# Optimization experiments

Hardware: AMD Instinct MI355X
Metric: run time of the kernel (lower is better)

## Reference

```python
import jax, jax.numpy as jnp
import numpy as np

IN_CH = 512
HID = 512
SCALE = 1.0 / np.sqrt(16.0)  # hard-coded 16**0.5 in source, not sqrt(hidden)


def setup_inputs() -> dict:
    key = jax.random.key(0)
    ks = jax.random.split(key, 9)
    B, T = 8, 2048
    lim = 1.0 / np.sqrt(IN_CH)
    return {
        "q": jax.random.normal(ks[0], (B, T, IN_CH), dtype=jnp.float32),
        "k": jax.random.normal(ks[1], (B, T, IN_CH), dtype=jnp.float32),
        "v": jax.random.normal(ks[2], (B, T, IN_CH), dtype=jnp.float32),
        "Wq": jax.random.uniform(ks[3], (IN_CH, HID), jnp.float32, -lim, lim),
        "bq": jax.random.uniform(ks[4], (HID,), jnp.float32, -lim, lim),
        "Wk": jax.random.uniform(ks[5], (IN_CH, HID), jnp.float32, -lim, lim),
        "bk": jax.random.uniform(ks[6], (HID,), jnp.float32, -lim, lim),
        "Wv": jax.random.uniform(ks[7], (IN_CH, HID), jnp.float32, -lim, lim),
        "bv": jax.random.uniform(ks[8], (HID,), jnp.float32, -lim, lim),
    }


def reference(q, k, v, Wq, bq, Wk, bk, Wv, bv):
    # Linear projections: [B,T,F] @ [F,H] + [H]
    query = jnp.einsum("btf,fh->bth", q, Wq) + bq
    key_p = jnp.einsum("btf,fh->bth", k, Wk) + bk
    value = jnp.einsum("btf,fh->bth", v, Wv) + bv
    # energy: [B,T,T], scaled by fixed 1/sqrt(16)
    energy = jnp.einsum("bth,bsh->bts", query, key_p) * SCALE
    attn = jax.nn.softmax(energy, axis=-1)
    # weighted sum: [B,T,H]
    return jnp.einsum("bts,bsh->bth", attn, value)
```

## Files before the change

### kernel.cpp

```cpp
#include <hip/hip_runtime.h>
#include <stdint.h>

typedef __bf16 bf16;
typedef bf16 bf16x8 __attribute__((ext_vector_type(8)));
typedef float f32x4 __attribute__((ext_vector_type(4)));

#define MFMA(a, b, c) __builtin_amdgcn_mfma_f32_16x16x32_bf16(a, b, c, 0, 0, 0)

#define SCALE_L2E 0.3606737602222409f
#define M0 16.0f

__device__ __forceinline__ void gload_lds16(const void* g, void* l) {
  __builtin_amdgcn_global_load_lds(
      (const __attribute__((address_space(1))) uint32_t*)g,
      (__attribute__((address_space(3))) uint32_t*)l, 16, 0, 0);
}

__global__ void k_wtrans(const float* __restrict__ Wq, const float* __restrict__ Wk,
                         const float* __restrict__ Wv, bf16* __restrict__ Wt) {
  __shared__ float tile[32][33];
  int x = threadIdx.x, y = threadIdx.y;
  int k0 = blockIdx.x * 32, n0 = blockIdx.y * 32, z = blockIdx.z;
  const float* W = (z == 0) ? Wq : (z == 1) ? Wk : Wv;
  for (int j = 0; j < 4; j++)
    tile[y + 8 * j][x] = W[(size_t)(k0 + y + 8 * j) * 512 + n0 + x];
  __syncthreads();
  bf16* o = Wt + (size_t)z * 262144;
  for (int j = 0; j < 4; j++)
    o[(size_t)(n0 + y + 8 * j) * 512 + k0 + x] = (bf16)tile[x][y + 8 * j];
}

__global__ __launch_bounds__(256, 3) void k_proj(
    const float* __restrict__ q, const float* __restrict__ k, const float* __restrict__ v,
    const bf16* __restrict__ Wt, const float* __restrict__ bq, const float* __restrict__ bk,
    const float* __restrict__ bv, bf16* __restrict__ Qp, bf16* __restrict__ Kp,
    bf16* __restrict__ Vtp) {
  int z = blockIdx.z;
  const float* A = (z == 0) ? q : (z == 1) ? k : v;
  const float* bias = (z == 0) ? bq : (z == 1) ? bk : bv;
  const bf16* Bw = Wt + (size_t)z * 262144;

  int m0 = blockIdx.x * 128, n0 = blockIdx.y * 128;
  __shared__ __align__(16) char smem[34816];
  bf16* As = (bf16*)smem;
  bf16* Bs = (bf16*)(smem + 18432);
  bf16* Ts = (bf16*)smem;

  int tid = threadIdx.x;
  int wave = tid >> 6, lane = tid & 63, qr = lane & 15, quad = lane >> 4;
  int wm = (wave >> 1) * 64, wn = (wave & 1) * 64;

  f32x4 acc[4][4];
  for (int mi = 0; mi < 4; mi++)
    for (int ni = 0; ni < 4; ni++) acc[mi][ni] = (f32x4){0.f, 0.f, 0.f, 0.f};

  for (int k0 = 0; k0 < 512; k0 += 64) {
    __syncthreads();
    for (int i = 0; i < 4; i++) {
      int ch = i * 256 + tid;
      int row = ch >> 3, c = ch & 7;
      int cs = c ^ (row & 7);
      gload_lds16(Bw + (size_t)(n0 + row) * 512 + k0 + cs * 8, &Bs[ch * 8]);
      const float4* src = (const float4*)(A + (size_t)(m0 + row) * 512 + k0 + c * 8);
      float4 x = src[0], y = src[1];
      bf16x8 t;
      t[0] = (bf16)x.x; t[1] = (bf16)x.y; t[2] = (bf16)x.z; t[3] = (bf16)x.w;
      t[4] = (bf16)y.x; t[5] = (bf16)y.y; t[6] = (bf16)y.z; t[7] = (bf16)y.w;
      *(bf16x8*)&As[row * 72 + c * 8] = t;
    }
    __syncthreads();
    for (int h = 0; h < 2; h++) {
      bf16x8 af[4], bfv[4];
      for (int mi = 0; mi < 4; mi++)
        af[mi] = *(bf16x8*)&As[(wm + mi * 16 + qr) * 72 + h * 32 + quad * 8];
      for (int ni = 0; ni < 4; ni++) {
        int rr = wn + ni * 16 + qr;
        int cc = (h * 4 + quad) ^ (rr & 7);
        bfv[ni] = *(bf16x8*)&Bs[rr * 64 + cc * 8];
      }
      for (int mi = 0; mi < 4; mi++)
        for (int ni = 0; ni < 4; ni++) acc[mi][ni] = MFMA(af[mi], bfv[ni], acc[mi][ni]);
    }
  }

  if (z == 2) {
    __syncthreads();
    for (int ni = 0; ni < 4; ni++) {
      int hcol = wn + ni * 16 + qr;
      float bz = bias[n0 + hcol];
      for (int mi = 0; mi < 4; mi++) {
        int tl = wm + mi * 16 + quad * 4;
        bf16 tmp[4];
        for (int r = 0; r < 4; r++) tmp[r] = (bf16)(acc[mi][ni][r] + bz);
        *(uint64_t*)&Ts[hcol * 136 + tl] = *(uint64_t*)tmp;
      }
    }
    __syncthreads();
    int bb = m0 >> 11, t0l = m0 & 2047;
    for (int i = 0; i < 8; i++) {
      int ch = i * 256 + tid;
      int row = ch >> 4, c = ch & 15;
      *(bf16x8*)(Vtp + (size_t)(bb * 512 + n0 + row) * 2048 + t0l + c * 8) =
          *(bf16x8*)&Ts[row * 136 + c * 8];
    }
  } else {
    bf16* C = (z == 0) ? Qp : Kp;
    float sc = (z == 0) ? SCALE_L2E : 1.0f;
    for (int ni = 0; ni < 4; ni++) {
      int col = n0 + wn + ni * 16 + qr;
      float bz = bias[col];
      for (int mi = 0; mi < 4; mi++) {
        int rbase = m0 + wm + mi * 16 + quad * 4;
        for (int r = 0; r < 4; r++)
          C[(size_t)(rbase + r) * 512 + col] = (bf16)((acc[mi][ni][r] + bz) * sc);
      }
    }
  }
}

__global__ __launch_bounds__(256, 3) void k_qk(const bf16* __restrict__ Qp,
                                               const bf16* __restrict__ Kp,
                                               bf16* __restrict__ P,
                                               float* __restrict__ Lpart) {
  __shared__ bf16 As[128 * 64];
  __shared__ bf16 Bs[128 * 64];
  int b = blockIdx.z;
  const bf16* A = Qp + (size_t)b * 2048 * 512;
  const bf16* B = Kp + (size_t)b * 2048 * 512;
  bf16* Pb = P + (size_t)b * 2048 * 2048;
  int m0 = blockIdx.x * 128, n0 = blockIdx.y * 128;
  int tid = threadIdx.x;
  int wave = tid >> 6, lane = tid & 63, qr = lane & 15, quad = lane >> 4;
  int wm = (wave >> 1) * 64, wn = (wave & 1) * 64;

  f32x4 acc[4][4];
  for (int mi = 0; mi < 4; mi++)
    for (int ni = 0; ni < 4; ni++) acc[mi][ni] = (f32x4){0.f, 0.f, 0.f, 0.f};

  for (int k0 = 0; k0 < 512; k0 += 64) {
    __syncthreads();
    for (int i = 0; i < 4; i++) {
      int ch = i * 256 + tid;
      int row = ch >> 3, c = ch & 7;
      int cs = c ^ (row & 7);
      gload_lds16(A + (size_t)(m0 + row) * 512 + k0 + cs * 8, &As[ch * 8]);
      gload_lds16(B + (size_t)(n0 + row) * 512 + k0 + cs * 8, &Bs[ch * 8]);
    }
    __syncthreads();
    for (int h = 0; h < 2; h++) {
      bf16x8 af[4], bfv[4];
      for (int mi = 0; mi < 4; mi++) {
        int rr = wm + mi * 16 + qr;
        int cc = (h * 4 + quad) ^ (rr & 7);
        af[mi] = *(bf16x8*)&As[rr * 64 + cc * 8];
      }
      for (int ni = 0; ni < 4; ni++) {
        int rr = wn + ni * 16 + qr;
        int cc = (h * 4 + quad) ^ (rr & 7);
        bfv[ni] = *(bf16x8*)&Bs[rr * 64 + cc * 8];
      }
      for (int mi = 0; mi < 4; mi++)
        for (int ni = 0; ni < 4; ni++) acc[mi][ni] = MFMA(af[mi], bfv[ni], acc[mi][ni]);
    }
  }

  int slice = blockIdx.y * 2 + (wave & 1);
  float* Lp = Lpart + (size_t)slice * 16384 + b * 2048;
  for (int mi = 0; mi < 4; mi++) {
    int rowb = m0 + wm + mi * 16 + quad * 4;
    for (int r = 0; r < 4; r++) {
      float s = 0.f;
      bf16* prow = Pb + (size_t)(rowb + r) * 2048 + n0 + wn + qr;
      for (int ni = 0; ni < 4; ni++) {
        float e = exp2f(acc[mi][ni][r] - M0);
        prow[ni * 16] = (bf16)e;
        s += e;
      }
      s += __shfl_xor(s, 1);
      s += __shfl_xor(s, 2);
      s += __shfl_xor(s, 4);
      s += __shfl_xor(s, 8);
      if (qr == 0) Lp[rowb + r] = s;
    }
  }
}

__global__ __launch_bounds__(256, 3) void k_pv(const bf16* __restrict__ P,
                                               const bf16* __restrict__ Vtp,
                                               const float* __restrict__ Lpart,
                                               float* __restrict__ out) {
  __shared__ bf16 As[128 * 64];
  __shared__ bf16 Bs[128 * 64];
  __shared__ float Linv_s[128];
  int b = blockIdx.z;
  const bf16* A = P + (size_t)b * 2048 * 2048;
  const bf16* B = Vtp + (size_t)b * 512 * 2048;
  int m0 = blockIdx.x * 128, n0 = blockIdx.y * 128;
  int tid = threadIdx.x;
  int wave = tid >> 6, lane = tid & 63, qr = lane & 15, quad = lane >> 4;
  int wm = (wave >> 1) * 64, wn = (wave & 1) * 64;

  if (tid < 128) {
    float s = 0.f;
    for (int j = 0; j < 32; j++) s += Lpart[(size_t)j * 16384 + b * 2048 + m0 + tid];
    Linv_s[tid] = 1.0f / s;
  }

  f32x4 acc[4][4];
  for (int mi = 0; mi < 4; mi++)
    for (int ni = 0; ni < 4; ni++) acc[mi][ni] = (f32x4){0.f, 0.f, 0.f, 0.f};

  for (int k0 = 0; k0 < 2048; k0 += 64) {
    __syncthreads();
    for (int i = 0; i < 4; i++) {
      int ch = i * 256 + tid;
      int row = ch >> 3, c = ch & 7;
      int cs = c ^ (row & 7);
      gload_lds16(A + (size_t)(m0 + row) * 2048 + k0 + cs * 8, &As[ch * 8]);
      gload_lds16(B + (size_t)(n0 + row) * 2048 + k0 + cs * 8, &Bs[ch * 8]);
    }
    __syncthreads();
    for (int h = 0; h < 2; h++) {
      bf16x8 af[4], bfv[4];
      for (int mi = 0; mi < 4; mi++) {
        int rr = wm + mi * 16 + qr;
        int cc = (h * 4 + quad) ^ (rr & 7);
        af[mi] = *(bf16x8*)&As[rr * 64 + cc * 8];
      }
      for (int ni = 0; ni < 4; ni++) {
        int rr = wn + ni * 16 + qr;
        int cc = (h * 4 + quad) ^ (rr & 7);
        bfv[ni] = *(bf16x8*)&Bs[rr * 64 + cc * 8];
      }
      for (int mi = 0; mi < 4; mi++)
        for (int ni = 0; ni < 4; ni++) acc[mi][ni] = MFMA(af[mi], bfv[ni], acc[mi][ni]);
    }
  }

  for (int mi = 0; mi < 4; mi++) {
    int rowl = wm + mi * 16 + quad * 4;
    float linv[4];
    for (int r = 0; r < 4; r++) linv[r] = Linv_s[rowl + r];
    for (int ni = 0; ni < 4; ni++) {
      int col = n0 + wn + ni * 16 + qr;
      float* og = out + (size_t)(b * 2048 + m0 + rowl) * 512 + col;
      for (int r = 0; r < 4; r++) og[(size_t)r * 512] = acc[mi][ni][r] * linv[r];
    }
  }
}

extern "C" void kernel_launch(void* const* d_in, const int* in_sizes, int n_in,
                              void* d_out, int out_size, void* d_ws, size_t ws_size,
                              hipStream_t stream) {
  (void)in_sizes; (void)n_in; (void)out_size; (void)ws_size;
  const float* q  = (const float*)d_in[0];
  const float* k  = (const float*)d_in[1];
  const float* v  = (const float*)d_in[2];
  const float* Wq = (const float*)d_in[3];
  const float* bq = (const float*)d_in[4];
  const float* Wk = (const float*)d_in[5];
  const float* bk = (const float*)d_in[6];
  const float* Wv = (const float*)d_in[7];
  const float* bv = (const float*)d_in[8];
  float* out = (float*)d_out;

  char* ws = (char*)d_ws;
  bf16* Wt     = (bf16*)(ws);
  bf16* Qp     = (bf16*)(ws + 1572864);
  bf16* Kp     = (bf16*)(ws + 18350080);
  bf16* Vtp    = (bf16*)(ws + 35127296);
  bf16* P      = (bf16*)(ws + 51904512);
  float* Lpart = (float*)(ws + 119013376);

  k_wtrans<<<dim3(16, 16, 3), dim3(32, 8, 1), 0, stream>>>(Wq, Wk, Wv, Wt);
  k_proj<<<dim3(128, 4, 3), 256, 0, stream>>>(q, k, v, Wt, bq, bk, bv, Qp, Kp, Vtp);
  k_qk<<<dim3(16, 16, 8), 256, 0, stream>>>(Qp, Kp, P, Lpart);
  k_pv<<<dim3(16, 4, 8), 256, 0, stream>>>(P, Vtp, Lpart, out);
}
```

Before: 275.1 us.

## Double-buffer LDS tiles in projection, QK and PV GEMM kernels

Converts the three GEMM kernels from single-buffered load-then-compute loops into double-buffered pipelines. The next K tile is prefetched into the alternate LDS buffer (and into registers for the fp32 A operand in the projection) while MFMAs run on the current one, which halves barriers per iteration. The projection A tile moves from a padded layout to an XOR-swizzled one, and the Linv staging reuses the A buffer after the loop. LDS use doubles, so launch bounds drop from 3 to 2 blocks per CU, trading occupancy for overlap.

```diff
diff --git a/kernel.cpp b/kernel.cpp
--- a/kernel.cpp
+++ b/kernel.cpp
@@ -30,7 +30,7 @@
     o[(size_t)(n0 + y + 8 * j) * 512 + k0 + x] = (bf16)tile[x][y + 8 * j];
 }
 
-__global__ __launch_bounds__(256, 3) void k_proj(
+__global__ __launch_bounds__(256, 2) void k_proj(
     const float* __restrict__ q, const float* __restrict__ k, const float* __restrict__ v,
     const bf16* __restrict__ Wt, const float* __restrict__ bq, const float* __restrict__ bk,
     const float* __restrict__ bv, bf16* __restrict__ Qp, bf16* __restrict__ Kp,
@@ -41,9 +41,9 @@
   const bf16* Bw = Wt + (size_t)z * 262144;
 
   int m0 = blockIdx.x * 128, n0 = blockIdx.y * 128;
-  __shared__ __align__(16) char smem[34816];
+  __shared__ __align__(16) char smem[65536];
   bf16* As = (bf16*)smem;
-  bf16* Bs = (bf16*)(smem + 18432);
+  bf16* Bs = (bf16*)(smem + 32768);
   bf16* Ts = (bf16*)smem;
 
   int tid = threadIdx.x;
@@ -54,37 +54,73 @@
   for (int mi = 0; mi < 4; mi++)
     for (int ni = 0; ni < 4; ni++) acc[mi][ni] = (f32x4){0.f, 0.f, 0.f, 0.f};
 
-  for (int k0 = 0; k0 < 512; k0 += 64) {
-    __syncthreads();
-    for (int i = 0; i < 4; i++) {
-      int ch = i * 256 + tid;
-      int row = ch >> 3, c = ch & 7;
-      int cs = c ^ (row & 7);
-      gload_lds16(Bw + (size_t)(n0 + row) * 512 + k0 + cs * 8, &Bs[ch * 8]);
-      const float4* src = (const float4*)(A + (size_t)(m0 + row) * 512 + k0 + c * 8);
-      float4 x = src[0], y = src[1];
+  float4 rx[4], ry[4];
+
+  auto issue = [&](int kk, int buf) {
+#pragma unroll
+    for (int i = 0; i < 4; i++) {
+      int ch = i * 256 + tid, row = ch >> 3, c = ch & 7;
+      const float4* src = (const float4*)(A + (size_t)(m0 + row) * 512 + kk + c * 8);
+      rx[i] = src[0];
+      ry[i] = src[1];
+    }
+#pragma unroll
+    for (int i = 0; i < 4; i++) {
+      int ch = i * 256 + tid, row = ch >> 3, c = ch & 7, cs = c ^ (row & 7);
+      gload_lds16(Bw + (size_t)(n0 + row) * 512 + kk + cs * 8, &Bs[buf * 8192 + ch * 8]);
+    }
+  };
+
+  auto writeA = [&](int buf) {
+#pragma unroll
+    for (int i = 0; i < 4; i++) {
+      int ch = i * 256 + tid, row = ch >> 3, c = ch & 7, cs = c ^ (row & 7);
       bf16x8 t;
-      t[0] = (bf16)x.x; t[1] = (bf16)x.y; t[2] = (bf16)x.z; t[3] = (bf16)x.w;
-      t[4] = (bf16)y.x; t[5] = (bf16)y.y; t[6] = (bf16)y.z; t[7] = (bf16)y.w;
-      *(bf16x8*)&As[row * 72 + c * 8] = t;
-    }
-    __syncthreads();
+      t[0] = (bf16)rx[i].x; t[1] = (bf16)rx[i].y; t[2] = (bf16)rx[i].z; t[3] = (bf16)rx[i].w;
+      t[4] = (bf16)ry[i].x; t[5] = (bf16)ry[i].y; t[6] = (bf16)ry[i].z; t[7] = (bf16)ry[i].w;
+      *(bf16x8*)&As[buf * 8192 + row * 64 + cs * 8] = t;
+    }
+  };
+
+  auto compute = [&](int buf) {
+    bf16* Ab = &As[buf * 8192];
+    bf16* Bb = &Bs[buf * 8192];
+#pragma unroll
     for (int h = 0; h < 2; h++) {
       bf16x8 af[4], bfv[4];
-      for (int mi = 0; mi < 4; mi++)
-        af[mi] = *(bf16x8*)&As[(wm + mi * 16 + qr) * 72 + h * 32 + quad * 8];
+#pragma unroll
+      for (int mi = 0; mi < 4; mi++) {
+        int rr = wm + mi * 16 + qr;
+        int cc = (h * 4 + quad) ^ (rr & 7);
+        af[mi] = *(bf16x8*)&Ab[rr * 64 + cc * 8];
+      }
+#pragma unroll
       for (int ni = 0; ni < 4; ni++) {
         int rr = wn + ni * 16 + qr;
         int cc = (h * 4 + quad) ^ (rr & 7);
-        bfv[ni] = *(bf16x8*)&Bs[rr * 64 + cc * 8];
-      }
+        bfv[ni] = *(bf16x8*)&Bb[rr * 64 + cc * 8];
+      }
+#pragma unroll
       for (int mi = 0; mi < 4; mi++)
+#pragma unroll
         for (int ni = 0; ni < 4; ni++) acc[mi][ni] = MFMA(af[mi], bfv[ni], acc[mi][ni]);
     }
+  };
+
+  issue(0, 0);
+  writeA(0);
+  __syncthreads();
+
+  int cur = 0;
+  for (int t = 0; t < 8; t++) {
+    if (t < 7) issue((t + 1) * 64, cur ^ 1);
+    compute(cur);
+    if (t < 7) writeA(cur ^ 1);
+    __syncthreads();
+    cur ^= 1;
   }
 
   if (z == 2) {
-    __syncthreads();
     for (int ni = 0; ni < 4; ni++) {
       int hcol = wn + ni * 16 + qr;
       float bz = bias[n0 + hcol];
@@ -118,12 +154,12 @@
   }
 }
 
-__global__ __launch_bounds__(256, 3) void k_qk(const bf16* __restrict__ Qp,
+__global__ __launch_bounds__(256, 2) void k_qk(const bf16* __restrict__ Qp,
                                                const bf16* __restrict__ Kp,
                                                bf16* __restrict__ P,
                                                float* __restrict__ Lpart) {
-  __shared__ bf16 As[128 * 64];
-  __shared__ bf16 Bs[128 * 64];
+  __shared__ bf16 As[2][128 * 64];
+  __shared__ bf16 Bs[2][128 * 64];
   int b = blockIdx.z;
   const bf16* A = Qp + (size_t)b * 2048 * 512;
   const bf16* B = Kp + (size_t)b * 2048 * 512;
@@ -137,31 +173,46 @@
   for (int mi = 0; mi < 4; mi++)
     for (int ni = 0; ni < 4; ni++) acc[mi][ni] = (f32x4){0.f, 0.f, 0.f, 0.f};
 
-  for (int k0 = 0; k0 < 512; k0 += 64) {
-    __syncthreads();
-    for (int i = 0; i < 4; i++) {
-      int ch = i * 256 + tid;
-      int row = ch >> 3, c = ch & 7;
-      int cs = c ^ (row & 7);
-      gload_lds16(A + (size_t)(m0 + row) * 512 + k0 + cs * 8, &As[ch * 8]);
-      gload_lds16(B + (size_t)(n0 + row) * 512 + k0 + cs * 8, &Bs[ch * 8]);
-    }
-    __syncthreads();
+  auto stage = [&](int kk, int buf) {
+#pragma unroll
+    for (int i = 0; i < 4; i++) {
+      int ch = i * 256 + tid, row = ch >> 3, c = ch & 7, cs = c ^ (row & 7);
+      gload_lds16(A + (size_t)(m0 + row) * 512 + kk + cs * 8, &As[buf][ch * 8]);
+      gload_lds16(B + (size_t)(n0 + row) * 512 + kk + cs * 8, &Bs[buf][ch * 8]);
+    }
+  };
+
+  auto compute = [&](int buf) {
+#pragma unroll
     for (int h = 0; h < 2; h++) {
       bf16x8 af[4], bfv[4];
+#pragma unroll
       for (int mi = 0; mi < 4; mi++) {
         int rr = wm + mi * 16 + qr;
         int cc = (h * 4 + quad) ^ (rr & 7);
-        af[mi] = *(bf16x8*)&As[rr * 64 + cc * 8];
-      }
+        af[mi] = *(bf16x8*)&As[buf][rr * 64 + cc * 8];
+      }
+#pragma unroll
       for (int ni = 0; ni < 4; ni++) {
         int rr = wn + ni * 16 + qr;
         int cc = (h * 4 + quad) ^ (rr & 7);
-        bfv[ni] = *(bf16x8*)&Bs[rr * 64 + cc * 8];
-      }
+        bfv[ni] = *(bf16x8*)&Bs[buf][rr * 64 + cc * 8];
+      }
+#pragma unroll
       for (int mi = 0; mi < 4; mi++)
+#pragma unroll
         for (int ni = 0; ni < 4; ni++) acc[mi][ni] = MFMA(af[mi], bfv[ni], acc[mi][ni]);
     }
+  };
+
+  stage(0, 0);
+  __syncthreads();
+  int cur = 0;
+  for (int t = 0; t < 8; t++) {
+    if (t < 7) stage((t + 1) * 64, cur ^ 1);
+    compute(cur);
+    __syncthreads();
+    cur ^= 1;
   }
 
   int slice = blockIdx.y * 2 + (wave & 1);
@@ -185,13 +236,12 @@
   }
 }
 
-__global__ __launch_bounds__(256, 3) void k_pv(const bf16* __restrict__ P,
+__global__ __launch_bounds__(256, 2) void k_pv(const bf16* __restrict__ P,
                                                const bf16* __restrict__ Vtp,
                                                const float* __restrict__ Lpart,
                                                float* __restrict__ out) {
-  __shared__ bf16 As[128 * 64];
-  __shared__ bf16 Bs[128 * 64];
-  __shared__ float Linv_s[128];
+  __shared__ bf16 As[2][128 * 64];
+  __shared__ bf16 Bs[2][128 * 64];
   int b = blockIdx.z;
   const bf16* A = P + (size_t)b * 2048 * 2048;
   const bf16* B = Vtp + (size_t)b * 512 * 2048;
@@ -200,42 +250,62 @@
   int wave = tid >> 6, lane = tid & 63, qr = lane & 15, quad = lane >> 4;
   int wm = (wave >> 1) * 64, wn = (wave & 1) * 64;
 
+  float linv_own = 0.f;
   if (tid < 128) {
     float s = 0.f;
     for (int j = 0; j < 32; j++) s += Lpart[(size_t)j * 16384 + b * 2048 + m0 + tid];
-    Linv_s[tid] = 1.0f / s;
+    linv_own = 1.0f / s;
   }
 
   f32x4 acc[4][4];
   for (int mi = 0; mi < 4; mi++)
     for (int ni = 0; ni < 4; ni++) acc[mi][ni] = (f32x4){0.f, 0.f, 0.f, 0.f};
 
-  for (int k0 = 0; k0 < 2048; k0 += 64) {
-    __syncthreads();
-    for (int i = 0; i < 4; i++) {
-      int ch = i * 256 + tid;
-      int row = ch >> 3, c = ch & 7;
-      int cs = c ^ (row & 7);
-      gload_lds16(A + (size_t)(m0 + row) * 2048 + k0 + cs * 8, &As[ch * 8]);
-      gload_lds16(B + (size_t)(n0 + row) * 2048 + k0 + cs * 8, &Bs[ch * 8]);
-    }
-    __syncthreads();
+  auto stage = [&](int kk, int buf) {
+#pragma unroll
+    for (int i = 0; i < 4; i++) {
+      int ch = i * 256 + tid, row = ch >> 3, c = ch & 7, cs = c ^ (row & 7);
+      gload_lds16(A + (size_t)(m0 + row) * 2048 + kk + cs * 8, &As[buf][ch * 8]);
+      gload_lds16(B + (size_t)(n0 + row) * 2048 + kk + cs * 8, &Bs[buf][ch * 8]);
+    }
+  };
+
+  auto compute = [&](int buf) {
+#pragma unroll
     for (int h = 0; h < 2; h++) {
       bf16x8 af[4], bfv[4];
+#pragma unroll
       for (int mi = 0; mi < 4; mi++) {
         int rr = wm + mi * 16 + qr;
         int cc = (h * 4 + quad) ^ (rr & 7);
-        af[mi] = *(bf16x8*)&As[rr * 64 + cc * 8];
-      }
+        af[mi] = *(bf16x8*)&As[buf][rr * 64 + cc * 8];
+      }
+#pragma unroll
       for (int ni = 0; ni < 4; ni++) {
         int rr = wn + ni * 16 + qr;
         int cc = (h * 4 + quad) ^ (rr & 7);
-        bfv[ni] = *(bf16x8*)&Bs[rr * 64 + cc * 8];
-      }
+        bfv[ni] = *(bf16x8*)&Bs[buf][rr * 64 + cc * 8];
+      }
+#pragma unroll
       for (int mi = 0; mi < 4; mi++)
+#pragma unroll
         for (int ni = 0; ni < 4; ni++) acc[mi][ni] = MFMA(af[mi], bfv[ni], acc[mi][ni]);
     }
-  }
+  };
+
+  stage(0, 0);
+  __syncthreads();
+  int cur = 0;
+  for (int t = 0; t < 32; t++) {
+    if (t < 31) stage((t + 1) * 64, cur ^ 1);
+    compute(cur);
+    __syncthreads();
+    cur ^= 1;
+  }
+
+  float* Linv_s = (float*)&As[0][0];
+  if (tid < 128) Linv_s[tid] = linv_own;
+  __syncthreads();
 
   for (int mi = 0; mi < 4; mi++) {
     int rowl = wm + mi * 16 + quad * 4;
```

Result: no change. 278.8 us (+1.4%).
